# Optimization experiments

Hardware: AMD Instinct MI355X
Metric: run time of the kernel (lower is better)

Reference implementation:

```python
import jax, jax.numpy as jnp
import numpy as np

TOP_K = 2


def setup_inputs() -> dict:
    key = jax.random.key(0)
    ks = jax.random.split(key, 5)
    B, S, H, E, F = 2, 4096, 2048, 8, 4096
    scale_h = 1.0 / np.sqrt(H)
    scale_f = 1.0 / np.sqrt(F)
    return {
        "hidden_states": jax.random.normal(ks[0], (B, S, H), jnp.float32),
        "gate_w": jax.random.normal(ks[1], (E, H), jnp.float32) * scale_h,
        "w1": jax.random.normal(ks[2], (E, F, H), jnp.float32) * scale_h,
        "w3": jax.random.normal(ks[3], (E, F, H), jnp.float32) * scale_h,
        "w2": jax.random.normal(ks[4], (E, H, F), jnp.float32) * scale_f,
    }


def reference(hidden_states, gate_w, w1, w3, w2):
    B, S, H = hidden_states.shape
    E = gate_w.shape[0]
    x = hidden_states.reshape(-1, H)                      # [T, H]
    T = x.shape[0]

    # Router: logits -> softmax(fp32) -> top-k -> renormalize
    router_logits = x @ gate_w.T                          # [T, E]
    probs = jax.nn.softmax(router_logits.astype(jnp.float32), axis=-1)
    topk_w, topk_idx = jax.lax.top_k(probs, TOP_K)        # [T, k]
    topk_w = topk_w / jnp.sum(topk_w, axis=-1, keepdims=True)
    topk_w = topk_w.astype(x.dtype)

    # Per-expert combine weight (0 for unselected experts) [T, E]
    combine = jnp.sum(jax.nn.one_hot(topk_idx, E, dtype=x.dtype)
                      * topk_w[..., None], axis=1)

    # Expert SwiGLU MLPs, weighted-accumulated (loop over fixed E=8)
    out = jnp.zeros((T, H), dtype=x.dtype)
    for e in range(E):
        h = jax.nn.silu(x @ w1[e].T) * (x @ w3[e].T)      # [T, F]
        out = out + (h @ w2[e].T) * combine[:, e:e + 1]   # [T, H]

    return out.reshape(B, S, H), router_logits
```

## Files before the change

kernel.cpp:

```cpp
#include <hip/hip_runtime.h>
#include <math.h>

#define T_TOK 8192
#define H_DIM 2048
#define F_DIM 4096
#define E_NUM 8
#define MAXPAIR (T_TOK * 2)
#define MAX_MT 136
#define BM 128
#define BN 128
#define BK 32
#define NCONV 2048
#define NCONV13 4096

typedef __attribute__((ext_vector_type(4))) float f32x4;
typedef __attribute__((ext_vector_type(8))) short s16x8;
typedef __attribute__((ext_vector_type(8))) __bf16 bf16x8;
typedef __attribute__((ext_vector_type(4))) unsigned short u16x4;

__device__ __forceinline__ unsigned short f2bf(float f) {
  unsigned int u = __float_as_uint(f);
  u += 0x7FFFu + ((u >> 16) & 1u);
  return (unsigned short)(u >> 16);
}

__device__ __forceinline__ s16x8 pack8(f32x4 a, f32x4 b) {
  s16x8 r;
  r[0] = (short)f2bf(a.x); r[1] = (short)f2bf(a.y);
  r[2] = (short)f2bf(a.z); r[3] = (short)f2bf(a.w);
  r[4] = (short)f2bf(b.x); r[5] = (short)f2bf(b.y);
  r[6] = (short)f2bf(b.z); r[7] = (short)f2bf(b.w);
  return r;
}

#define GLD16(gsrc, ldst)                                                      \
  __builtin_amdgcn_global_load_lds(                                            \
      (__attribute__((address_space(1))) void*)(gsrc),                         \
      (__attribute__((address_space(3))) void*)(ldst), 16, 0, 0)

__global__ __launch_bounds__(256) void router_conv_kernel(
    const float* __restrict__ x, const float* __restrict__ gw,
    float* __restrict__ logits, unsigned short* __restrict__ xb,
    int* __restrict__ ctrl, int* __restrict__ tIdx, float* __restrict__ tW,
    const float* __restrict__ w1f, unsigned short* __restrict__ w1b,
    const float* __restrict__ w3f, unsigned short* __restrict__ w3b,
    int nconv) {
  int rb = blockIdx.x;
  if (nconv) {
    const int bid = blockIdx.x;
    if ((bid % 3) != 2) {
      const int cid = bid - (bid + 1) / 3;
      const float* src = (cid < 2048) ? w1f : w3f;
      unsigned short* dst = (cid < 2048) ? w1b : w3b;
      const long long base = (long long)(cid & 2047) * 4096;
#pragma unroll
      for (int it = 0; it < 16; ++it) {
        const long long i = base + it * 256 + threadIdx.x;
        f32x4 a = *(const f32x4*)(src + i * 8);
        f32x4 b = *(const f32x4*)(src + i * 8 + 4);
        *(s16x8*)(dst + i * 8) = pack8(a, b);
      }
      return;
    }
    rb = bid / 3;
  }

  const int wid = threadIdx.x >> 6, lane = threadIdx.x & 63;
  const int t = rb * 4 + wid;
  const float* xr = x + (size_t)t * H_DIM;
  float acc[E_NUM];
#pragma unroll
  for (int e = 0; e < E_NUM; ++e) acc[e] = 0.f;
#pragma unroll
  for (int c = 0; c < H_DIM / 256; ++c) {
    const int h0 = c * 256 + lane * 4;
    f32x4 xv = *(const f32x4*)(xr + h0);
    u16x4 p;
    p.x = f2bf(xv.x); p.y = f2bf(xv.y); p.z = f2bf(xv.z); p.w = f2bf(xv.w);
    *(u16x4*)(xb + (size_t)t * H_DIM + h0) = p;
#pragma unroll
    for (int e = 0; e < E_NUM; ++e) {
      f32x4 gv = *(const f32x4*)(gw + (size_t)e * H_DIM + h0);
      acc[e] += xv.x * gv.x + xv.y * gv.y + xv.z * gv.z + xv.w * gv.w;
    }
  }
#pragma unroll
  for (int e = 0; e < E_NUM; ++e) {
#pragma unroll
    for (int off = 32; off >= 1; off >>= 1) acc[e] += __shfl_xor(acc[e], off, 64);
  }
  if (lane == 0) {
#pragma unroll
    for (int e = 0; e < E_NUM; ++e) logits[(size_t)t * E_NUM + e] = acc[e];
    int i0 = 0;
    float m0 = acc[0];
    for (int e = 1; e < E_NUM; ++e)
      if (acc[e] > m0) { m0 = acc[e]; i0 = e; }
    int i1 = -1;
    float m1 = -3.4e38f;
    for (int e = 0; e < E_NUM; ++e)
      if (e != i0 && acc[e] > m1) { m1 = acc[e]; i1 = e; }
    float ex = expf(m1 - m0);
    float w0 = 1.f / (1.f + ex);
    float w1 = ex * w0;
    tIdx[t * 2] = i0; tIdx[t * 2 + 1] = i1;
    tW[t * 2] = w0;  tW[t * 2 + 1] = w1;
    atomicAdd(&ctrl[i0], 1);
    atomicAdd(&ctrl[i1], 1);
  }
}

__global__ __launch_bounds__(256) void plan_kernel(int* __restrict__ ctrl) {
  __shared__ int cnt[E_NUM], offs[E_NUM + 1], tbase[E_NUM + 1];
  const int t = threadIdx.x;
  if (t < E_NUM) cnt[t] = ctrl[t];
  __syncthreads();
  if (t == 0) {
    int off = 0, mt = 0;
    for (int e = 0; e < E_NUM; ++e) {
      offs[e] = off; tbase[e] = mt;
      ctrl[8 + e] = off;
      ctrl[16 + e] = off;
      off += cnt[e];
      mt += (cnt[e] + BM - 1) / BM;
    }
    offs[E_NUM] = off; tbase[E_NUM] = mt;
    ctrl[24] = mt;
  }
  __syncthreads();
  const int total = tbase[E_NUM];
  for (int i = t; i < total; i += 256) {
    int e = 0;
    while (tbase[e + 1] <= i) ++e;
    ctrl[32 + i] = e;
    ctrl[32 + MAX_MT + i] = offs[e] + (i - tbase[e]) * BM;
  }
}

__global__ __launch_bounds__(256) void scatter_kernel(
    const int* __restrict__ tIdx, const float* __restrict__ tW,
    int* __restrict__ ctrl, int* __restrict__ pairTok,
    float* __restrict__ pairWgt) {
  const int t = blockIdx.x * 256 + threadIdx.x;
  if (t >= T_TOK) return;
#pragma unroll
  for (int j = 0; j < 2; ++j) {
    const int e = tIdx[t * 2 + j];
    const int pos = atomicAdd(&ctrl[16 + e], 1);
    pairTok[pos] = t;
    pairWgt[pos] = tW[t * 2 + j];
  }
}

template <int BBF>
__global__ __launch_bounds__(256, 2) void gemm1_kernel(
    const float* __restrict__ w1f, const float* __restrict__ w3f,
    const unsigned short* __restrict__ w1b,
    const unsigned short* __restrict__ w3b,
    const unsigned short* __restrict__ xb, const int* __restrict__ ctrl,
    const int* __restrict__ pairTok, unsigned short* __restrict__ hbuf,
    const float* __restrict__ w2f, unsigned short* __restrict__ w2b,
    int nconv) {
  int gid = blockIdx.x;
  const int nconv3 = nconv * 3;
  if (gid < nconv3) {
    if ((gid % 3) == 2) {
      const int cid = gid / 3;
      const long long per = (long long)E_NUM * F_DIM * H_DIM / 8 / NCONV;
      long long i = (long long)cid * per + threadIdx.x;
      const long long end = (long long)(cid + 1) * per;
      for (; i < end; i += 256) {
        f32x4 a = *(const f32x4*)(w2f + i * 8);
        f32x4 b = *(const f32x4*)(w2f + i * 8 + 4);
        *(s16x8*)(w2b + i * 8) = pack8(a, b);
      }
      return;
    }
    gid = gid - (gid + 1) / 3;
  } else {
    gid = gid - nconv;
  }

  const int mtTotal = ctrl[24];
  const int mt = gid >> 5;
  const int nt = gid & 31;
  if (mt >= mtTotal) return;
  const int e = ctrl[32 + mt];
  const int mbase = ctrl[32 + MAX_MT + mt];
  int mValid = ctrl[8 + e] + ctrl[e] - mbase;
  if (mValid > BM) mValid = BM;
  const int nbase = nt * BN;

  __shared__ __align__(16) short sA[3][BM * BK];
  __shared__ __align__(16) short sB1[3][BM * BK];
  __shared__ __align__(16) short sB3[3][BM * BK];
  __shared__ int sTok[BM];

  const int tid = threadIdx.x;
  if (tid < BM) sTok[tid] = pairTok[mbase + (tid < mValid ? tid : 0)];
  __syncthreads();

  const int c0 = tid, c1 = tid + 256;
  const int r0 = c0 >> 2, r1 = c1 >> 2;
  const int kg0 = (c0 & 3) ^ ((r0 >> 1) & 3);
  const int kg1 = (c1 & 3) ^ ((r1 >> 1) & 3);

  const unsigned short* srcA0 = xb + (size_t)sTok[r0] * H_DIM + kg0 * 8;
  const unsigned short* srcA1 = xb + (size_t)sTok[r1] * H_DIM + kg1 * 8;
  const size_t wbase = (size_t)e * F_DIM * H_DIM;
  const float *f10, *f11, *f30, *f31;
  const unsigned short *p10, *p11, *p30, *p31;
  if constexpr (BBF) {
    p10 = w1b + wbase + (size_t)(nbase + r0) * H_DIM + kg0 * 8;
    p11 = w1b + wbase + (size_t)(nbase + r1) * H_DIM + kg1 * 8;
    p30 = w3b + wbase + (size_t)(nbase + r0) * H_DIM + kg0 * 8;
    p31 = w3b + wbase + (size_t)(nbase + r1) * H_DIM + kg1 * 8;
  } else {
    f10 = w1f + wbase + (size_t)(nbase + r0) * H_DIM + kg0 * 8;
    f11 = w1f + wbase + (size_t)(nbase + r1) * H_DIM + kg1 * 8;
    f30 = w3f + wbase + (size_t)(nbase + r0) * H_DIM + kg0 * 8;
    f31 = w3f + wbase + (size_t)(nbase + r1) * H_DIM + kg1 * 8;
  }

  f32x4 acc1[4][4], acc3[4][4];
  const f32x4 fz = {0.f, 0.f, 0.f, 0.f};
#pragma unroll
  for (int i = 0; i < 4; ++i)
#pragma unroll
    for (int j = 0; j < 4; ++j) { acc1[i][j] = fz; acc3[i][j] = fz; }

  const int lane = tid & 63, wid = tid >> 6;
  const int wm = (wid >> 1) * 64, wn = (wid & 1) * 64;
  const int rl = lane & 15, kq = lane >> 4;

  int aIdx[4], bIdx[4];
#pragma unroll
  for (int i = 0; i < 4; ++i) {
    const int ra = wm + i * 16 + rl;
    aIdx[i] = ra * BK + ((kq ^ ((ra >> 1) & 3)) * 8);
    const int rb = wn + i * 16 + rl;
    bIdx[i] = rb * BK + ((kq ^ ((rb >> 1) & 3)) * 8);
  }

#define STAGE1(buf, k0)                                                        \
  {                                                                            \
    GLD16(srcA0 + (k0), &sA[buf][c0 * 8]);                                     \
    GLD16(srcA1 + (k0), &sA[buf][c1 * 8]);                                     \
    if constexpr (BBF) {                                                       \
      GLD16(p10 + (k0), &sB1[buf][c0 * 8]);                                    \
      GLD16(p11 + (k0), &sB1[buf][c1 * 8]);                                    \
      GLD16(p30 + (k0), &sB3[buf][c0 * 8]);                                    \
      GLD16(p31 + (k0), &sB3[buf][c1 * 8]);                                    \
    } else {                                                                   \
      f32x4 t0 = *(const f32x4*)(f10 + (k0));                                  \
      f32x4 t1 = *(const f32x4*)(f10 + (k0) + 4);                              \
      *(s16x8*)&sB1[buf][c0 * 8] = pack8(t0, t1);                              \
      t0 = *(const f32x4*)(f11 + (k0));                                        \
      t1 = *(const f32x4*)(f11 + (k0) + 4);                                    \
      *(s16x8*)&sB1[buf][c1 * 8] = pack8(t0, t1);                              \
      t0 = *(const f32x4*)(f30 + (k0));                                        \
      t1 = *(const f32x4*)(f30 + (k0) + 4);                                    \
      *(s16x8*)&sB3[buf][c0 * 8] = pack8(t0, t1);                              \
      t0 = *(const f32x4*)(f31 + (k0));                                        \
      t1 = *(const f32x4*)(f31 + (k0) + 4);                                    \
      *(s16x8*)&sB3[buf][c1 * 8] = pack8(t0, t1);                              \
    }                                                                          \
  }

  STAGE1(0, 0);
  STAGE1(1, BK);
  if constexpr (BBF)
    asm volatile("s_waitcnt vmcnt(6)" ::: "memory");
  else
    asm volatile("s_waitcnt vmcnt(0) lgkmcnt(0)" ::: "memory");
  __builtin_amdgcn_s_barrier();
  asm volatile("" ::: "memory");

  const int NS = H_DIM / BK;
  int cur = 0;
  for (int s = 0; s < NS; ++s) {
    if (s + 2 < NS) {
      const int nxt = (cur + 2 >= 3) ? cur - 1 : cur + 2;
      STAGE1(nxt, (s + 2) * BK);
    }
    asm volatile("" ::: "memory");

    bf16x8 af[4], bf1[4], bf3[4];
#pragma unroll
    for (int i = 0; i < 4; ++i) {
      af[i] = *(const bf16x8*)&sA[cur][aIdx[i]];
      bf1[i] = *(const bf16x8*)&sB1[cur][bIdx[i]];
      bf3[i] = *(const bf16x8*)&sB3[cur][bIdx[i]];
    }
    __builtin_amdgcn_s_setprio(1);
#pragma unroll
    for (int mr = 0; mr < 4; ++mr)
#pragma unroll
      for (int nr = 0; nr < 4; ++nr) {
        acc1[mr][nr] = __builtin_amdgcn_mfma_f32_16x16x32_bf16(
            af[mr], bf1[nr], acc1[mr][nr], 0, 0, 0);
        acc3[mr][nr] = __builtin_amdgcn_mfma_f32_16x16x32_bf16(
            af[mr], bf3[nr], acc3[mr][nr], 0, 0, 0);
      }
    __builtin_amdgcn_s_setprio(0);
    asm volatile("" ::: "memory");

    if (s + 1 < NS) {
      if constexpr (BBF) {
        if (s + 2 < NS)
          asm volatile("s_waitcnt vmcnt(6)" ::: "memory");
        else
          asm volatile("s_waitcnt vmcnt(0)" ::: "memory");
      } else {
        asm volatile("s_waitcnt vmcnt(0) lgkmcnt(0)" ::: "memory");
      }
      __builtin_amdgcn_s_barrier();
      asm volatile("" ::: "memory");
    }
    cur = (cur + 1 >= 3) ? 0 : cur + 1;
  }

#pragma unroll
  for (int mr = 0; mr < 4; ++mr) {
#pragma unroll
    for (int j = 0; j < 4; ++j) {
      const int row = wm + mr * 16 + kq * 4 + j;
      if (row < mValid) {
        unsigned short* dst =
            hbuf + (size_t)(mbase + row) * F_DIM + nbase + wn + rl;
#pragma unroll
        for (int nr = 0; nr < 4; ++nr) {
          const float z = acc1[mr][nr][j];
          const float hv = (z / (1.f + expf(-z))) * acc3[mr][nr][j];
          dst[nr * 16] = f2bf(hv);
        }
      }
    }
  }
#undef STAGE1
}

template <int BBF>
__global__ __launch_bounds__(256, 2) void gemm2_kernel(
    const float* __restrict__ w2f, const unsigned short* __restrict__ w2b,
    const unsigned short* __restrict__ hbuf, const int* __restrict__ ctrl,
    const int* __restrict__ pairTok, const float* __restrict__ pairWgt,
    float* __restrict__ out) {
  const int mtTotal = ctrl[24];
  const int mt = (blockIdx.x >> 7) * 8 + (blockIdx.x & 7);
  const int nt = (blockIdx.x >> 3) & 15;
  if (mt >= mtTotal) return;
  const int e = ctrl[32 + mt];
  const int mbase = ctrl[32 + MAX_MT + mt];
  int mValid = ctrl[8 + e] + ctrl[e] - mbase;
  if (mValid > BM) mValid = BM;
  const int nbase = nt * BN;

  __shared__ __align__(16) short sA[3][BM * BK];
  __shared__ __align__(16) short sB[3][BM * BK];
  __shared__ int sTok[BM];
  __shared__ float sWgt[BM];

  const int tid = threadIdx.x;
  if (tid < BM) {
    const int p = mbase + (tid < mValid ? tid : 0);
    sTok[tid] = pairTok[p];
    sWgt[tid] = pairWgt[p];
  }
  __syncthreads();

  const int c0 = tid, c1 = tid + 256;
  const int r0 = c0 >> 2, r1 = c1 >> 2;
  const int kg0 = (c0 & 3) ^ ((r0 >> 1) & 3);
  const int kg1 = (c1 & 3) ^ ((r1 >> 1) & 3);

  size_t pa0 = (size_t)(mbase + r0); if (pa0 > MAXPAIR - 1) pa0 = MAXPAIR - 1;
  size_t pa1 = (size_t)(mbase + r1); if (pa1 > MAXPAIR - 1) pa1 = MAXPAIR - 1;
  const unsigned short* srcA0 = hbuf + pa0 * F_DIM + kg0 * 8;
  const unsigned short* srcA1 = hbuf + pa1 * F_DIM + kg1 * 8;
  const size_t wbase = (size_t)e * H_DIM * F_DIM;
  const float *fw0, *fw1;
  const unsigned short *pw0, *pw1;
  if constexpr (BBF) {
    pw0 = w2b + wbase + (size_t)(nbase + r0) * F_DIM + kg0 * 8;
    pw1 = w2b + wbase + (size_t)(nbase + r1) * F_DIM + kg1 * 8;
  } else {
    fw0 = w2f + wbase + (size_t)(nbase + r0) * F_DIM + kg0 * 8;
    fw1 = w2f + wbase + (size_t)(nbase + r1) * F_DIM + kg1 * 8;
  }

  f32x4 acc[4][4];
  const f32x4 fz = {0.f, 0.f, 0.f, 0.f};
#pragma unroll
  for (int i = 0; i < 4; ++i)
#pragma unroll
    for (int j = 0; j < 4; ++j) acc[i][j] = fz;

  const int lane = tid & 63, wid = tid >> 6;
  const int wm = (wid >> 1) * 64, wn = (wid & 1) * 64;
  const int rl = lane & 15, kq = lane >> 4;

  int aIdx[4], bIdx[4];
#pragma unroll
  for (int i = 0; i < 4; ++i) {
    const int ra = wm + i * 16 + rl;
    aIdx[i] = ra * BK + ((kq ^ ((ra >> 1) & 3)) * 8);
    const int rb = wn + i * 16 + rl;
    bIdx[i] = rb * BK + ((kq ^ ((rb >> 1) & 3)) * 8);
  }

#define STAGE2(buf, k0)                                                        \
  {                                                                            \
    GLD16(srcA0 + (k0), &sA[buf][c0 * 8]);                                     \
    GLD16(srcA1 + (k0), &sA[buf][c1 * 8]);                                     \
    if constexpr (BBF) {                                                       \
      GLD16(pw0 + (k0), &sB[buf][c0 * 8]);                                     \
      GLD16(pw1 + (k0), &sB[buf][c1 * 8]);                                     \
    } else {                                                                   \
      f32x4 t0 = *(const f32x4*)(fw0 + (k0));                                  \
      f32x4 t1 = *(const f32x4*)(fw0 + (k0) + 4);                              \
      *(s16x8*)&sB[buf][c0 * 8] = pack8(t0, t1);                               \
      t0 = *(const f32x4*)(fw1 + (k0));                                        \
      t1 = *(const f32x4*)(fw1 + (k0) + 4);                                    \
      *(s16x8*)&sB[buf][c1 * 8] = pack8(t0, t1);                               \
    }                                                                          \
  }

  STAGE2(0, 0);
  STAGE2(1, BK);
  if constexpr (BBF)
    asm volatile("s_waitcnt vmcnt(4)" ::: "memory");
  else
    asm volatile("s_waitcnt vmcnt(0) lgkmcnt(0)" ::: "memory");
  __builtin_amdgcn_s_barrier();
  asm volatile("" ::: "memory");

  const int NS = F_DIM / BK;
  int cur = 0;
  for (int s = 0; s < NS; ++s) {
    if (s + 2 < NS) {
      const int nxt = (cur + 2 >= 3) ? cur - 1 : cur + 2;
      STAGE2(nxt, (s + 2) * BK);
    }
    asm volatile("" ::: "memory");

    bf16x8 af[4], bf[4];
#pragma unroll
    for (int i = 0; i < 4; ++i) {
      af[i] = *(const bf16x8*)&sA[cur][aIdx[i]];
      bf[i] = *(const bf16x8*)&sB[cur][bIdx[i]];
    }
    __builtin_amdgcn_s_setprio(1);
#pragma unroll
    for (int mr = 0; mr < 4; ++mr)
#pragma unroll
      for (int nr = 0; nr < 4; ++nr)
        acc[mr][nr] = __builtin_amdgcn_mfma_f32_16x16x32_bf16(
            af[mr], bf[nr], acc[mr][nr], 0, 0, 0);
    __builtin_amdgcn_s_setprio(0);
    asm volatile("" ::: "memory");

    if (s + 1 < NS) {
      if constexpr (BBF) {
        if (s + 2 < NS)
          asm volatile("s_waitcnt vmcnt(4)" ::: "memory");
        else
          asm volatile("s_waitcnt vmcnt(0)" ::: "memory");
      } else {
        asm volatile("s_waitcnt vmcnt(0) lgkmcnt(0)" ::: "memory");
      }
      __builtin_amdgcn_s_barrier();
      asm volatile("" ::: "memory");
    }
    cur = (cur + 1 >= 3) ? 0 : cur + 1;
  }

#pragma unroll
  for (int mr = 0; mr < 4; ++mr) {
#pragma unroll
    for (int j = 0; j < 4; ++j) {
      const int row = wm + mr * 16 + kq * 4 + j;
      if (row < mValid) {
        const int tok = sTok[row];
        const float w = sWgt[row];
        float* dst = out + (size_t)tok * H_DIM + nbase + wn + rl;
#pragma unroll
        for (int nr = 0; nr < 4; ++nr)
          unsafeAtomicAdd(dst + nr * 16, w * acc[mr][nr][j]);
      }
    }
  }
#undef STAGE2
}

extern "C" void kernel_launch(void* const* d_in, const int* in_sizes, int n_in,
                              void* d_out, int out_size, void* d_ws,
                              size_t ws_size, hipStream_t stream) {
  const float* x  = (const float*)d_in[0];
  const float* gw = (const float*)d_in[1];
  const float* w1 = (const float*)d_in[2];
  const float* w3 = (const float*)d_in[3];
  const float* w2 = (const float*)d_in[4];
  float* out = (float*)d_out;
  float* logits = out + (size_t)T_TOK * H_DIM;

  char* ws = (char*)d_ws;
  const size_t HDR = 1u << 20;
  const size_t XB_SZ = (size_t)T_TOK * H_DIM * 2;
  const size_t HB_SZ = (size_t)MAXPAIR * F_DIM * 2;
  const size_t W_SZ  = (size_t)E_NUM * F_DIM * H_DIM * 2;

  int* ctrl = (int*)(ws);
  int* tIdx = (int*)(ws + 4096);
  float* tW = (float*)(ws + 4096 + 65536);
  int* pairTok = (int*)(ws + 4096 + 131072);
  float* pairWgt = (float*)(ws + 4096 + 196608);
  unsigned short* xb = (unsigned short*)(ws + HDR);
  unsigned short* hbuf = (unsigned short*)(ws + HDR + XB_SZ);
  unsigned short* w1b = (unsigned short*)(ws + HDR + XB_SZ + HB_SZ);
  unsigned short* w3b = w1b + W_SZ / 2;
  unsigned short* w2b = w3b + W_SZ / 2;

  const bool cw13 = ws_size >= HDR + XB_SZ + HB_SZ + 2 * W_SZ;
  const bool cw2  = ws_size >= HDR + XB_SZ + HB_SZ + 3 * W_SZ;

  hipMemsetAsync(ctrl, 0, 4096, stream);
  hipMemsetAsync(out, 0, (size_t)T_TOK * H_DIM * sizeof(float), stream);

  if (cw13)
    router_conv_kernel<<<6144, 256, 0, stream>>>(
        x, gw, logits, xb, ctrl, tIdx, tW, w1, w1b, w3, w3b, NCONV13);
  else
    router_conv_kernel<<<T_TOK / 4, 256, 0, stream>>>(
        x, gw, logits, xb, ctrl, tIdx, tW, w1, w1b, w3, w3b, 0);

  plan_kernel<<<1, 256, 0, stream>>>(ctrl);
  scatter_kernel<<<T_TOK / 256, 256, 0, stream>>>(tIdx, tW, ctrl, pairTok, pairWgt);

  const int NG = MAX_MT * 32;
  if (cw13) {
    const int nconv = cw2 ? NCONV : 0;
    gemm1_kernel<1><<<NG + nconv, 256, 0, stream>>>(
        w1, w3, w1b, w3b, xb, ctrl, pairTok, hbuf, w2, w2b, nconv);
  } else {
    gemm1_kernel<0><<<NG, 256, 0, stream>>>(
        w1, w3, w1b, w3b, xb, ctrl, pairTok, hbuf, w2, w2b, 0);
  }
  if (cw2)
    gemm2_kernel<1><<<MAX_MT * 16, 256, 0, stream>>>(w2, w2b, hbuf, ctrl,
                                                     pairTok, pairWgt, out);
  else
    gemm2_kernel<0><<<MAX_MT * 16, 256, 0, stream>>>(w2, w2b, hbuf, ctrl,
                                                     pairTok, pairWgt, out);
}
```

Before: 1.431 ms.

## Enlarge gemm1 M-tile to 256 rows with 512 threads and split-phase double buffering

The gate/up GEMM now uses 256-row token tiles with 512-thread blocks and its own tile plan in the control buffer. Each 128-column slab of w1/w3 is therefore loaded once per 256 tokens instead of once per 128. The 3-stage pipeline is replaced by a double buffer over 64-wide K steps, each split into two halves, with loads for A, B1 and B3 interleaved between the w1 and w3 MFMA groups. This cuts weight traffic and barrier count per FLOP. In exchange it uses more shared memory per block, doubles per-expert padding waste, and halves the number of tiles.

```diff
diff --git a/kernel.cpp b/kernel.cpp
--- a/kernel.cpp
+++ b/kernel.cpp
@@ -7,7 +7,9 @@
 #define E_NUM 8
 #define MAXPAIR (T_TOK * 2)
 #define MAX_MT 136
+#define MAX_MT2 72
 #define BM 128
+#define BM1 256
 #define BN 128
 #define BK 32
 #define NCONV 2048
@@ -111,29 +113,36 @@
 }
 
 __global__ __launch_bounds__(256) void plan_kernel(int* __restrict__ ctrl) {
-  __shared__ int cnt[E_NUM], offs[E_NUM + 1], tbase[E_NUM + 1];
+  __shared__ int cnt[E_NUM], offs[E_NUM + 1], tb1[E_NUM + 1], tb2[E_NUM + 1];
   const int t = threadIdx.x;
   if (t < E_NUM) cnt[t] = ctrl[t];
   __syncthreads();
   if (t == 0) {
-    int off = 0, mt = 0;
+    int off = 0, mt = 0, mt2 = 0;
     for (int e = 0; e < E_NUM; ++e) {
-      offs[e] = off; tbase[e] = mt;
+      offs[e] = off; tb1[e] = mt; tb2[e] = mt2;
       ctrl[8 + e] = off;
       ctrl[16 + e] = off;
+      mt += (cnt[e] + BM - 1) / BM;
+      mt2 += (cnt[e] + BM1 - 1) / BM1;
       off += cnt[e];
-      mt += (cnt[e] + BM - 1) / BM;
-    }
-    offs[E_NUM] = off; tbase[E_NUM] = mt;
+    }
+    offs[E_NUM] = off; tb1[E_NUM] = mt; tb2[E_NUM] = mt2;
     ctrl[24] = mt;
+    ctrl[25] = mt2;
   }
   __syncthreads();
-  const int total = tbase[E_NUM];
-  for (int i = t; i < total; i += 256) {
+  for (int i = t; i < tb1[E_NUM]; i += 256) {
     int e = 0;
-    while (tbase[e + 1] <= i) ++e;
+    while (tb1[e + 1] <= i) ++e;
     ctrl[32 + i] = e;
-    ctrl[32 + MAX_MT + i] = offs[e] + (i - tbase[e]) * BM;
+    ctrl[32 + MAX_MT + i] = offs[e] + (i - tb1[e]) * BM;
+  }
+  for (int i = t; i < tb2[E_NUM]; i += 256) {
+    int e = 0;
+    while (tb2[e + 1] <= i) ++e;
+    ctrl[304 + i] = e;
+    ctrl[384 + i] = offs[e] + (i - tb2[e]) * BM1;
   }
 }
 
@@ -153,7 +162,7 @@
 }
 
 template <int BBF>
-__global__ __launch_bounds__(256, 2) void gemm1_kernel(
+__global__ __launch_bounds__(512, 2) void gemm1_kernel(
     const float* __restrict__ w1f, const float* __restrict__ w3f,
     const unsigned short* __restrict__ w1b,
     const unsigned short* __restrict__ w3b,
@@ -169,7 +178,7 @@
       const long long per = (long long)E_NUM * F_DIM * H_DIM / 8 / NCONV;
       long long i = (long long)cid * per + threadIdx.x;
       const long long end = (long long)(cid + 1) * per;
-      for (; i < end; i += 256) {
+      for (; i < end; i += 512) {
         f32x4 a = *(const f32x4*)(w2f + i * 8);
         f32x4 b = *(const f32x4*)(w2f + i * 8 + 4);
         *(s16x8*)(w2b + i * 8) = pack8(a, b);
@@ -181,45 +190,43 @@
     gid = gid - nconv;
   }
 
-  const int mtTotal = ctrl[24];
+  const int mtTotal = ctrl[25];
   const int mt = gid >> 5;
   const int nt = gid & 31;
   if (mt >= mtTotal) return;
-  const int e = ctrl[32 + mt];
-  const int mbase = ctrl[32 + MAX_MT + mt];
+  const int e = ctrl[304 + mt];
+  const int mbase = ctrl[384 + mt];
   int mValid = ctrl[8 + e] + ctrl[e] - mbase;
-  if (mValid > BM) mValid = BM;
+  if (mValid > BM1) mValid = BM1;
   const int nbase = nt * BN;
 
-  __shared__ __align__(16) short sA[3][BM * BK];
-  __shared__ __align__(16) short sB1[3][BM * BK];
-  __shared__ __align__(16) short sB3[3][BM * BK];
-  __shared__ int sTok[BM];
+  __shared__ __align__(16) short sA[2][2][BM1 * 32];
+  __shared__ __align__(16) short sB1[2][2][BN * 32];
+  __shared__ __align__(16) short sB3[2][2][BN * 32];
+  __shared__ int sTok[BM1];
 
   const int tid = threadIdx.x;
-  if (tid < BM) sTok[tid] = pairTok[mbase + (tid < mValid ? tid : 0)];
+  if (tid < BM1) sTok[tid] = pairTok[mbase + (tid < mValid ? tid : 0)];
   __syncthreads();
 
-  const int c0 = tid, c1 = tid + 256;
-  const int r0 = c0 >> 2, r1 = c1 >> 2;
-  const int kg0 = (c0 & 3) ^ ((r0 >> 1) & 3);
-  const int kg1 = (c1 & 3) ^ ((r1 >> 1) & 3);
-
-  const unsigned short* srcA0 = xb + (size_t)sTok[r0] * H_DIM + kg0 * 8;
-  const unsigned short* srcA1 = xb + (size_t)sTok[r1] * H_DIM + kg1 * 8;
+  const int cA0 = tid, cA1 = tid + 512;
+  const int rA0 = cA0 >> 2, rA1 = cA1 >> 2;
+  const int kgA0 = (cA0 & 3) ^ ((rA0 >> 1) & 3);
+  const int kgA1 = (cA1 & 3) ^ ((rA1 >> 1) & 3);
+  const unsigned short* srcA0 = xb + (size_t)sTok[rA0] * H_DIM + kgA0 * 8;
+  const unsigned short* srcA1 = xb + (size_t)sTok[rA1] * H_DIM + kgA1 * 8;
+  const int cB = tid;
+  const int rB = cB >> 2;
+  const int kgB = (cB & 3) ^ ((rB >> 1) & 3);
   const size_t wbase = (size_t)e * F_DIM * H_DIM;
-  const float *f10, *f11, *f30, *f31;
-  const unsigned short *p10, *p11, *p30, *p31;
+  const float *f1p, *f3p;
+  const unsigned short *p1p, *p3p;
   if constexpr (BBF) {
-    p10 = w1b + wbase + (size_t)(nbase + r0) * H_DIM + kg0 * 8;
-    p11 = w1b + wbase + (size_t)(nbase + r1) * H_DIM + kg1 * 8;
-    p30 = w3b + wbase + (size_t)(nbase + r0) * H_DIM + kg0 * 8;
-    p31 = w3b + wbase + (size_t)(nbase + r1) * H_DIM + kg1 * 8;
+    p1p = w1b + wbase + (size_t)(nbase + rB) * H_DIM + kgB * 8;
+    p3p = w3b + wbase + (size_t)(nbase + rB) * H_DIM + kgB * 8;
   } else {
-    f10 = w1f + wbase + (size_t)(nbase + r0) * H_DIM + kg0 * 8;
-    f11 = w1f + wbase + (size_t)(nbase + r1) * H_DIM + kg1 * 8;
-    f30 = w3f + wbase + (size_t)(nbase + r0) * H_DIM + kg0 * 8;
-    f31 = w3f + wbase + (size_t)(nbase + r1) * H_DIM + kg1 * 8;
+    f1p = w1f + wbase + (size_t)(nbase + rB) * H_DIM + kgB * 8;
+    f3p = w3f + wbase + (size_t)(nbase + rB) * H_DIM + kgB * 8;
   }
 
   f32x4 acc1[4][4], acc3[4][4];
@@ -230,94 +237,126 @@
     for (int j = 0; j < 4; ++j) { acc1[i][j] = fz; acc3[i][j] = fz; }
 
   const int lane = tid & 63, wid = tid >> 6;
-  const int wm = (wid >> 1) * 64, wn = (wid & 1) * 64;
+  const int wm = (wid >> 1) * 64;
+  const int wn = (wid & 1) * 64;
   const int rl = lane & 15, kq = lane >> 4;
 
   int aIdx[4], bIdx[4];
 #pragma unroll
   for (int i = 0; i < 4; ++i) {
     const int ra = wm + i * 16 + rl;
-    aIdx[i] = ra * BK + ((kq ^ ((ra >> 1) & 3)) * 8);
+    aIdx[i] = ra * 32 + ((kq ^ ((ra >> 1) & 3)) * 8);
     const int rb = wn + i * 16 + rl;
-    bIdx[i] = rb * BK + ((kq ^ ((rb >> 1) & 3)) * 8);
-  }
-
-#define STAGE1(buf, k0)                                                        \
+    bIdx[i] = rb * 32 + ((kq ^ ((rb >> 1) & 3)) * 8);
+  }
+
+#define ST_A(buf, h, koff)                                                     \
   {                                                                            \
-    GLD16(srcA0 + (k0), &sA[buf][c0 * 8]);                                     \
-    GLD16(srcA1 + (k0), &sA[buf][c1 * 8]);                                     \
+    GLD16(srcA0 + (koff), &sA[buf][h][cA0 * 8]);                               \
+    GLD16(srcA1 + (koff), &sA[buf][h][cA1 * 8]);                               \
+  }
+#define ST_B(buf, h, koff)                                                     \
+  {                                                                            \
     if constexpr (BBF) {                                                       \
-      GLD16(p10 + (k0), &sB1[buf][c0 * 8]);                                    \
-      GLD16(p11 + (k0), &sB1[buf][c1 * 8]);                                    \
-      GLD16(p30 + (k0), &sB3[buf][c0 * 8]);                                    \
-      GLD16(p31 + (k0), &sB3[buf][c1 * 8]);                                    \
+      GLD16(p1p + (koff), &sB1[buf][h][cB * 8]);                               \
+      GLD16(p3p + (koff), &sB3[buf][h][cB * 8]);                               \
     } else {                                                                   \
-      f32x4 t0 = *(const f32x4*)(f10 + (k0));                                  \
-      f32x4 t1 = *(const f32x4*)(f10 + (k0) + 4);                              \
-      *(s16x8*)&sB1[buf][c0 * 8] = pack8(t0, t1);                              \
-      t0 = *(const f32x4*)(f11 + (k0));                                        \
-      t1 = *(const f32x4*)(f11 + (k0) + 4);                                    \
-      *(s16x8*)&sB1[buf][c1 * 8] = pack8(t0, t1);                              \
-      t0 = *(const f32x4*)(f30 + (k0));                                        \
-      t1 = *(const f32x4*)(f30 + (k0) + 4);                                    \
-      *(s16x8*)&sB3[buf][c0 * 8] = pack8(t0, t1);                              \
-      t0 = *(const f32x4*)(f31 + (k0));                                        \
-      t1 = *(const f32x4*)(f31 + (k0) + 4);                                    \
-      *(s16x8*)&sB3[buf][c1 * 8] = pack8(t0, t1);                              \
+      f32x4 t0 = *(const f32x4*)(f1p + (koff));                                \
+      f32x4 t1 = *(const f32x4*)(f1p + (koff) + 4);                            \
+      *(s16x8*)&sB1[buf][h][cB * 8] = pack8(t0, t1);                           \
+      t0 = *(const f32x4*)(f3p + (koff));                                      \
+      t1 = *(const f32x4*)(f3p + (koff) + 4);                                  \
+      *(s16x8*)&sB3[buf][h][cB * 8] = pack8(t0, t1);                           \
     }                                                                          \
   }
-
-  STAGE1(0, 0);
-  STAGE1(1, BK);
-  if constexpr (BBF)
-    asm volatile("s_waitcnt vmcnt(6)" ::: "memory");
-  else
-    asm volatile("s_waitcnt vmcnt(0) lgkmcnt(0)" ::: "memory");
+#define WAITC1(N)                                                              \
+  {                                                                            \
+    if constexpr (BBF)                                                         \
+      asm volatile("s_waitcnt vmcnt(" #N ")" ::: "memory");                    \
+    else                                                                       \
+      asm volatile("s_waitcnt vmcnt(0) lgkmcnt(0)" ::: "memory");              \
+  }
+
+  ST_A(0, 0, 0);
+  ST_B(0, 0, 0);
+  ST_A(0, 1, 32);
+  ST_B(0, 1, 32);
+  WAITC1(4);
   __builtin_amdgcn_s_barrier();
   asm volatile("" ::: "memory");
 
-  const int NS = H_DIM / BK;
-  int cur = 0;
-  for (int s = 0; s < NS; ++s) {
-    if (s + 2 < NS) {
-      const int nxt = (cur + 2 >= 3) ? cur - 1 : cur + 2;
-      STAGE1(nxt, (s + 2) * BK);
-    }
-    asm volatile("" ::: "memory");
-
+  const int NT = H_DIM / 64;
+  for (int t = 0; t < NT; ++t) {
+    const int buf = t & 1, nb = buf ^ 1;
+    const bool pf = (t + 1 < NT);
+    const int kn = (t + 1) * 64;
+
+    if (pf) ST_A(nb, 0, kn);
+    asm volatile("" ::: "memory");
     bf16x8 af[4], bf1[4], bf3[4];
 #pragma unroll
     for (int i = 0; i < 4; ++i) {
-      af[i] = *(const bf16x8*)&sA[cur][aIdx[i]];
-      bf1[i] = *(const bf16x8*)&sB1[cur][bIdx[i]];
-      bf3[i] = *(const bf16x8*)&sB3[cur][bIdx[i]];
+      af[i] = *(const bf16x8*)&sA[buf][0][aIdx[i]];
+      bf1[i] = *(const bf16x8*)&sB1[buf][0][bIdx[i]];
     }
     __builtin_amdgcn_s_setprio(1);
 #pragma unroll
     for (int mr = 0; mr < 4; ++mr)
 #pragma unroll
-      for (int nr = 0; nr < 4; ++nr) {
+      for (int nr = 0; nr < 4; ++nr)
         acc1[mr][nr] = __builtin_amdgcn_mfma_f32_16x16x32_bf16(
             af[mr], bf1[nr], acc1[mr][nr], 0, 0, 0);
+    __builtin_amdgcn_s_setprio(0);
+    if (pf) ST_B(nb, 0, kn);
+    asm volatile("" ::: "memory");
+#pragma unroll
+    for (int i = 0; i < 4; ++i) bf3[i] = *(const bf16x8*)&sB3[buf][0][bIdx[i]];
+    __builtin_amdgcn_s_setprio(1);
+#pragma unroll
+    for (int mr = 0; mr < 4; ++mr)
+#pragma unroll
+      for (int nr = 0; nr < 4; ++nr)
         acc3[mr][nr] = __builtin_amdgcn_mfma_f32_16x16x32_bf16(
             af[mr], bf3[nr], acc3[mr][nr], 0, 0, 0);
-      }
     __builtin_amdgcn_s_setprio(0);
     asm volatile("" ::: "memory");
-
-    if (s + 1 < NS) {
-      if constexpr (BBF) {
-        if (s + 2 < NS)
-          asm volatile("s_waitcnt vmcnt(6)" ::: "memory");
-        else
-          asm volatile("s_waitcnt vmcnt(0)" ::: "memory");
-      } else {
-        asm volatile("s_waitcnt vmcnt(0) lgkmcnt(0)" ::: "memory");
-      }
+    if (pf) { WAITC1(4); } else { WAITC1(0); }
+    __builtin_amdgcn_s_barrier();
+    asm volatile("" ::: "memory");
+
+    if (pf) ST_A(nb, 1, kn + 32);
+    asm volatile("" ::: "memory");
+#pragma unroll
+    for (int i = 0; i < 4; ++i) {
+      af[i] = *(const bf16x8*)&sA[buf][1][aIdx[i]];
+      bf1[i] = *(const bf16x8*)&sB1[buf][1][bIdx[i]];
+    }
+    __builtin_amdgcn_s_setprio(1);
+#pragma unroll
+    for (int mr = 0; mr < 4; ++mr)
+#pragma unroll
+      for (int nr = 0; nr < 4; ++nr)
+        acc1[mr][nr] = __builtin_amdgcn_mfma_f32_16x16x32_bf16(
+            af[mr], bf1[nr], acc1[mr][nr], 0, 0, 0);
+    __builtin_amdgcn_s_setprio(0);
+    if (pf) ST_B(nb, 1, kn + 32);
+    asm volatile("" ::: "memory");
+#pragma unroll
+    for (int i = 0; i < 4; ++i) bf3[i] = *(const bf16x8*)&sB3[buf][1][bIdx[i]];
+    __builtin_amdgcn_s_setprio(1);
+#pragma unroll
+    for (int mr = 0; mr < 4; ++mr)
+#pragma unroll
+      for (int nr = 0; nr < 4; ++nr)
+        acc3[mr][nr] = __builtin_amdgcn_mfma_f32_16x16x32_bf16(
+            af[mr], bf3[nr], acc3[mr][nr], 0, 0, 0);
+    __builtin_amdgcn_s_setprio(0);
+    asm volatile("" ::: "memory");
+    if (pf) {
+      WAITC1(4);
       __builtin_amdgcn_s_barrier();
       asm volatile("" ::: "memory");
     }
-    cur = (cur + 1 >= 3) ? 0 : cur + 1;
   }
 
 #pragma unroll
@@ -337,7 +376,9 @@
       }
     }
   }
-#undef STAGE1
+#undef ST_A
+#undef ST_B
+#undef WAITC1
 }
 
 template <int BBF>
@@ -537,13 +578,12 @@
   plan_kernel<<<1, 256, 0, stream>>>(ctrl);
   scatter_kernel<<<T_TOK / 256, 256, 0, stream>>>(tIdx, tW, ctrl, pairTok, pairWgt);
 
-  const int NG = MAX_MT * 32;
   if (cw13) {
     const int nconv = cw2 ? NCONV : 0;
-    gemm1_kernel<1><<<NG + nconv, 256, 0, stream>>>(
+    gemm1_kernel<1><<<nconv ? 6144 : MAX_MT2 * 32, 512, 0, stream>>>(
         w1, w3, w1b, w3b, xb, ctrl, pairTok, hbuf, w2, w2b, nconv);
   } else {
-    gemm1_kernel<0><<<NG, 256, 0, stream>>>(
+    gemm1_kernel<0><<<MAX_MT2 * 32, 512, 0, stream>>>(
         w1, w3, w1b, w3b, xb, ctrl, pairTok, hbuf, w2, w2b, 0);
   }
   if (cw2)
```

Measured after the change: 1.505 ms. +5.2%, slower.
